# Performance work log

Measured on AMD Instinct MI355X. Metric: run time of the kernel, lower is better.

## Reference

```python
import jax, jax.numpy as jnp
import numpy as np

B, T, C, H, DH, L, V = 4096, 32, 384, 6, 64, 6, 80


def _ln(x, g, b):
    m = x.mean(-1, keepdims=True)
    v = ((x - m) ** 2).mean(-1, keepdims=True)
    return (x - m) / jnp.sqrt(v + 1e-5) * g + b


def setup_inputs() -> dict:
    key = jax.random.key(0)
    ks = jax.random.split(key, 12)
    n = lambda k, s: jax.random.normal(k, s, dtype=jnp.float32) * 0.02
    return dict(
        idx=jax.random.randint(ks[0], (B, T), 0, V),
        tok_emb=n(ks[1], (V, C)),
        pos_emb=n(ks[2], (T, C)),
        ln1_g=jnp.ones((L, C), jnp.float32), ln1_b=jnp.zeros((L, C), jnp.float32),
        Wq=n(ks[3], (L, H, C, DH)), Wk=n(ks[4], (L, H, C, DH)), Wv=n(ks[5], (L, H, C, DH)),
        Wo=n(ks[6], (L, C, C)), bo=jnp.zeros((L, C), jnp.float32),
        ln2_g=jnp.ones((L, C), jnp.float32), ln2_b=jnp.zeros((L, C), jnp.float32),
        W1=n(ks[7], (L, C, 4 * C)), b1=jnp.zeros((L, 4 * C), jnp.float32),
        W2=n(ks[8], (L, 4 * C, C)), b2=jnp.zeros((L, C), jnp.float32),
        lnf_g=jnp.ones((C,), jnp.float32), lnf_b=jnp.zeros((C,), jnp.float32),
        Wlm=n(ks[9], (C, V)), blm=jnp.zeros((V,), jnp.float32),
    )


def reference(idx, tok_emb, pos_emb, ln1_g, ln1_b, Wq, Wk, Wv, Wo, bo,
              ln2_g, ln2_b, W1, b1, W2, b2, lnf_g, lnf_b, Wlm, blm):
    # token + position embeddings
    x = tok_emb[idx] + pos_emb[None]  # [B, T, C]
    mask = jnp.tril(jnp.ones((T, T), dtype=bool))  # causal

    def block(x, p):
        l1g, l1b, wq, wk, wv, wo, b_o, l2g, l2b, w1, b_1, w2, b_2 = p
        h = _ln(x, l1g, l1b)
        q = jnp.einsum('btc,hcd->bhtd', h, wq)
        k = jnp.einsum('btc,hcd->bhtd', h, wk)
        v = jnp.einsum('btc,hcd->bhtd', h, wv)
        s = jnp.einsum('bhtd,bhsd->bhts', q, k) * (DH ** -0.5)
        s = jnp.where(mask, s, -jnp.inf)
        a = jax.nn.softmax(s, axis=-1)  # dropout is identity in eval
        o = jnp.einsum('bhts,bhsd->bhtd', a, v)
        o = o.transpose(0, 2, 1, 3).reshape(x.shape[0], T, C)  # concat heads
        x = x + o @ wo + b_o
        h2 = _ln(x, l2g, l2b)
        x = x + jax.nn.relu(h2 @ w1 + b_1) @ w2 + b_2
        return x, None

    params = (ln1_g, ln1_b, Wq, Wk, Wv, Wo, bo, ln2_g, ln2_b, W1, b1, W2, b2)
    x, _ = jax.lax.scan(block, x, params)
    x = _ln(x, lnf_g, lnf_b)
    return x @ Wlm + blm  # [B, T, V]
```

## Files before the change

kernel.cpp:

```cpp
#include <hip/hip_runtime.h>
#include <hip/hip_fp16.h>
#include <stdint.h>


typedef unsigned short u16;
typedef __bf16 bf16x8 __attribute__((ext_vector_type(8)));
typedef float f32x4 __attribute__((ext_vector_type(4)));
typedef float f32x4v __attribute__((ext_vector_type(4)));
typedef unsigned uint2v __attribute__((ext_vector_type(2)));

#define M_TOK 131072
#define CDIM  384
#define TT    32
#define HH    6
#define DHEAD 64
#define LLAY  6
#define VOCAB 80
#define FFDIM 1536
#define QKVN  1152

__device__ __forceinline__ float b2f(u16 v) {
    union { unsigned int u; float f; } x; x.u = ((unsigned int)v) << 16; return x.f;
}
__device__ __forceinline__ u16 f2b(float f) {
    union { float f; unsigned int u; } x; x.f = f;
    unsigned int r = (x.u + 0x7fffu + ((x.u >> 16) & 1u)) >> 16;
    return (u16)r;
}
__device__ __forceinline__ void gload16(const u16* g, u16* l) {
    __builtin_amdgcn_global_load_lds(
        (const __attribute__((address_space(1))) void*)g,
        (__attribute__((address_space(3))) void*)l,
        16, 0, 0);
}
__device__ __forceinline__ float load_in(const void* p, size_t i, int m) {
    if (m == 0) return ((const float*)p)[i];
    u16 v = ((const u16*)p)[i];
    if (m == 1) return b2f(v);
    __half h; *(u16*)&h = v; return __half2float(h);
}

__global__ void detect_dtype_kernel(const void* ln1g, int* flag) {
    if (threadIdx.x == 0 && blockIdx.x == 0) {
        unsigned w = *(const unsigned*)ln1g;
        int m = 0;
        if (w == 0x3F803F80u) m = 1;
        else if (w == 0x3C003C00u) m = 2;
        *flag = m;
    }
}

__global__ void cvt_kernel(const void* __restrict__ src, u16* __restrict__ dst,
                           unsigned n, const int* __restrict__ flag) {
    const int m = *flag;
    unsigned i = blockIdx.x * 256 + threadIdx.x;
    if (i < n) dst[i] = f2b(load_in(src, i, m));
}

__global__ void transpose_kernel(const void* __restrict__ src, u16* __restrict__ dst,
                                 int R, int Cc, unsigned total,
                                 const int* __restrict__ flag) {
    const int m = *flag;
    unsigned i = blockIdx.x * 256 + threadIdx.x;
    if (i >= total) return;
    unsigned c  = i % R;
    unsigned t2 = i / R;
    unsigned n  = t2 % Cc;
    unsigned l  = t2 / Cc;
    dst[i] = f2b(load_in(src, ((size_t)l * R + c) * Cc + n, m));
}

__global__ void pack_qkv_kernel(const void* __restrict__ Wq, const void* __restrict__ Wk,
                                const void* __restrict__ Wv, u16* __restrict__ dst,
                                const int* __restrict__ flag) {
    const int m = *flag;
    unsigned i = blockIdx.x * 256 + threadIdx.x;
    const unsigned total = (unsigned)LLAY * QKVN * CDIM;
    if (i >= total) return;
    unsigned c  = i % CDIM;
    unsigned t2 = i / CDIM;
    unsigned n  = t2 % QKVN;
    unsigned l  = t2 / QKVN;
    const void* W = (n < 384) ? Wq : (n < 768) ? Wk : Wv;
    unsigned nn = n % 384;
    unsigned hh = nn >> 6, d = nn & 63;
    dst[i] = f2b(load_in(W, (((size_t)l * HH + hh) * CDIM + c) * DHEAD + d, m));
}

__global__ void embed_kernel(const int* __restrict__ idx, const void* __restrict__ tok,
                             const void* __restrict__ pos, float* __restrict__ x,
                             unsigned rows0, const int* __restrict__ flag) {
    const int m = *flag;
    unsigned i = blockIdx.x * 256 + threadIdx.x;
    unsigned c  = i % CDIM;
    unsigned bt = i / CDIM + rows0;
    unsigned t  = bt & (TT - 1);
    int id = idx[bt];
    x[i] = load_in(tok, (size_t)id * CDIM + c, m) + load_in(pos, (size_t)t * CDIM + c, m);
}

__global__ __launch_bounds__(256) void ln_kernel(const float* __restrict__ x,
                                                 const u16* __restrict__ g,
                                                 const u16* __restrict__ b,
                                                 u16* __restrict__ out) {
    const unsigned row  = blockIdx.x * 4 + (threadIdx.x >> 6);
    const unsigned lane = threadIdx.x & 63;
    const float* xr = x + (size_t)row * CDIM;
    float v[6]; float s = 0.f, s2 = 0.f;
#pragma unroll
    for (int j = 0; j < 6; j++) { v[j] = xr[lane + j * 64]; s += v[j]; s2 += v[j] * v[j]; }
#pragma unroll
    for (int off = 32; off; off >>= 1) { s += __shfl_xor(s, off); s2 += __shfl_xor(s2, off); }
    float mean = s * (1.f / CDIM);
    float var  = fmaxf(s2 * (1.f / CDIM) - mean * mean, 0.f);
    float rstd = rsqrtf(var + 1e-5f);
    u16* orow = out + (size_t)row * CDIM;
#pragma unroll
    for (int j = 0; j < 6; j++) {
        unsigned c = lane + j * 64;
        orow[c] = f2b((v[j] - mean) * rstd * b2f(g[c]) + b2f(b[c]));
    }
}

template<bool WIDE, bool BIAS, bool RELU, bool RESID, bool NBOUND, bool FOUT>
__global__ __launch_bounds__(512, WIDE ? 4 : 6)
void gemm_kernel(const u16* __restrict__ A, const u16* __restrict__ Bt,
                 const u16* __restrict__ bias, const float* resid,
                 u16* __restrict__ Cb, float* Cf,
                 int N, int K, int nt) {
    constexpr int BN = WIDE ? 256 : 128;
    constexpr int NF = WIDE ? 4 : 2;
    constexpr int WC = BN / 4;
    constexpr int BI = BN / 64;
    __shared__ __align__(16) u16 smem[8192 + BN * 64];
    u16* As = smem;
    u16* Bs = smem + 8192;
    float* eps = (float*)smem;

    const int tid  = threadIdx.x;
    const int lane = tid & 63;
    const int w    = tid >> 6;
    const int quad = lane >> 4;
    const int l16  = lane & 15;
    const int wm = w >> 2, wn = w & 3;

    const int id = blockIdx.x;
    const int sgrp = id >> 3;
    const int mtile = (id & 7) + 8 * (sgrp / nt);
    const int ntile = sgrp % nt;
    const long m0 = (long)mtile * 128;
    const long n0 = (long)ntile * BN;

    const u16* Ag[2]; u16* ldsA[2];
    const u16* Bg[BI]; u16* ldsB[BI];
#pragma unroll
    for (int n = 0; n < 2; n++) {
        const int si  = w * 128 + n * 64 + lane;
        const int row = si >> 3;
        const int p   = si & 7;
        const int s   = p ^ (row & 7);
        Ag[n] = A + (size_t)(m0 + row) * K + s * 8;
        ldsA[n] = As + (size_t)(w * 128 + n * 64) * 8;
    }
#pragma unroll
    for (int n = 0; n < BI; n++) {
        const int si  = (w * BI + n) * 64 + lane;
        const int row = si >> 3;
        const int p   = si & 7;
        const int s   = p ^ (row & 7);
        long brow = n0 + row;
        if (NBOUND) brow = brow < N ? brow : N - 1;
        Bg[n] = Bt + (size_t)brow * K + s * 8;
        ldsB[n] = Bs + (size_t)((w * BI + n) * 64) * 8;
    }

    f32x4 acc[4][NF];
#pragma unroll
    for (int i = 0; i < 4; i++)
#pragma unroll
        for (int j = 0; j < NF; j++) acc[i][j] = f32x4{0.f, 0.f, 0.f, 0.f};

    for (int k0 = 0; k0 < K; k0 += 64) {
        __syncthreads();
#pragma unroll
        for (int n = 0; n < 2; n++)  gload16(Ag[n] + k0, ldsA[n]);
#pragma unroll
        for (int n = 0; n < BI; n++) gload16(Bg[n] + k0, ldsB[n]);
        __syncthreads();
#pragma unroll
        for (int k32 = 0; k32 < 2; k32++) {
            bf16x8 af[4], bfr[NF];
#pragma unroll
            for (int i = 0; i < 4; i++) {
                const int row = wm * 64 + i * 16 + l16;
                const int p   = (k32 * 4 + quad) ^ (row & 7);
                af[i] = *(const bf16x8*)(&As[row * 64 + p * 8]);
            }
#pragma unroll
            for (int j = 0; j < NF; j++) {
                const int row = wn * WC + j * 16 + l16;
                const int p   = (k32 * 4 + quad) ^ (row & 7);
                bfr[j] = *(const bf16x8*)(&Bs[row * 64 + p * 8]);
            }
#pragma unroll
            for (int i = 0; i < 4; i++)
#pragma unroll
                for (int j = 0; j < NF; j++)
                    acc[i][j] = __builtin_amdgcn_mfma_f32_16x16x32_bf16(af[i], bfr[j], acc[i][j], 0, 0, 0);
        }
    }

    float bv[NF];
#pragma unroll
    for (int j = 0; j < NF; j++) {
        if (BIAS) {
            int col = (int)n0 + wn * WC + j * 16 + l16;
            bv[j] = (!NBOUND || col < N) ? b2f(bias[col]) : 0.f;
        } else bv[j] = 0.f;
    }

    constexpr int SR  = WIDE ? 32 : 64;
    constexpr int NPH = 128 / SR;
    constexpr int IB  = SR / 16;
    constexpr int TPR = BN / 4;
    constexpr int RPP = 512 / TPR;
    const int cc = (tid & (TPR - 1)) * 4;
    const int rr = tid / TPR;
#pragma unroll
    for (int q = 0; q < NPH; q++) {
        __syncthreads();
        if (wm == (q * SR) / 64) {
            const int ibase = ((q * SR) % 64) / 16;
#pragma unroll
            for (int ii = 0; ii < IB; ii++)
#pragma unroll
                for (int j = 0; j < NF; j++) {
                    const int lr = ii * 16 + quad * 4;
                    const int lc = wn * WC + j * 16 + l16;
#pragma unroll
                    for (int r = 0; r < 4; r++) {
                        float v = acc[ibase + ii][j][r] + bv[j];
                        if (RELU) v = fmaxf(v, 0.f);
                        eps[(lr + r) * BN + lc] = v;
                    }
                }
        }
        __syncthreads();
        const long rowbase = m0 + q * SR;
#pragma unroll
        for (int p = 0; p < SR / RPP; p++) {
            const int lrow = p * RPP + rr;
            const long grow = rowbase + lrow;
            f32x4v v = *(const f32x4v*)&eps[lrow * BN + cc];
            const long col = n0 + cc;
            if (RESID) {
                if (!NBOUND || col + 3 < N) {
                    const f32x4v rv = *(const f32x4v*)&resid[grow * N + col];
                    v = v + rv;
                    __builtin_nontemporal_store(v, (f32x4v*)&Cf[grow * N + col]);
                }
            } else if (FOUT) {
                if (!NBOUND || col + 3 < N)
                    __builtin_nontemporal_store(v, (f32x4v*)&Cf[grow * N + col]);
            } else {
                if (!NBOUND || col + 3 < N) {
                    uint2v pk;
                    pk.x = (unsigned)f2b(v.x) | ((unsigned)f2b(v.y) << 16);
                    pk.y = (unsigned)f2b(v.z) | ((unsigned)f2b(v.w) << 16);
                    __builtin_nontemporal_store(pk, (uint2v*)&Cb[grow * N + col]);
                }
            }
        }
    }
}

__global__ __launch_bounds__(256, 2) void attn_kernel(const u16* __restrict__ qkv,
                                                      u16* __restrict__ o) {
    __shared__ __align__(16) u16 alds[4 * 3840];
    const int w    = threadIdx.x >> 6;
    u16* Pl = alds + w * 3840;
    u16* VT = Pl + 1280;

    const int gw   = blockIdx.x * 4 + w;
    const int seq  = gw / HH;
    const int h    = gw - seq * HH;
    const int lane = threadIdx.x & 63;
    const int l16  = lane & 15;
    const int quad = lane >> 4;

    const u16* base = qkv + (size_t)seq * TT * QKVN;
    const u16* Qb = base + h * DHEAD;
    const u16* Kb = base + 384 + h * DHEAD;
    const u16* Vb = base + 768 + h * DHEAD;

    {
        const int s  = lane & 31;
        const int hf = lane >> 5;
#pragma unroll
        for (int c = 0; c < 4; c++) {
            uint4 v = *(const uint4*)(Vb + (size_t)s * QKVN + hf * 32 + c * 8);
            const u16* pv = (const u16*)&v;
#pragma unroll
            for (int j = 0; j < 8; j++) {
                const int d = hf * 32 + c * 8 + j;
                VT[d * 40 + s] = pv[j];
            }
        }
    }

    bf16x8 qf[2][2], kf[2][2];
#pragma unroll
    for (int ti = 0; ti < 2; ti++)
#pragma unroll
        for (int kt = 0; kt < 2; kt++)
            qf[ti][kt] = *(const bf16x8*)(Qb + (size_t)(ti * 16 + l16) * QKVN + kt * 32 + quad * 8);
#pragma unroll
    for (int si = 0; si < 2; si++)
#pragma unroll
        for (int kt = 0; kt < 2; kt++)
            kf[si][kt] = *(const bf16x8*)(Kb + (size_t)(si * 16 + l16) * QKVN + kt * 32 + quad * 8);

    f32x4 S00 = f32x4{0.f, 0.f, 0.f, 0.f};
    f32x4 S10 = f32x4{0.f, 0.f, 0.f, 0.f};
    f32x4 S11 = f32x4{0.f, 0.f, 0.f, 0.f};
#pragma unroll
    for (int kt = 0; kt < 2; kt++) {
        S00 = __builtin_amdgcn_mfma_f32_16x16x32_bf16(qf[0][kt], kf[0][kt], S00, 0, 0, 0);
        S10 = __builtin_amdgcn_mfma_f32_16x16x32_bf16(qf[1][kt], kf[0][kt], S10, 0, 0, 0);
        S11 = __builtin_amdgcn_mfma_f32_16x16x32_bf16(qf[1][kt], kf[1][kt], S11, 0, 0, 0);
    }

#pragma unroll
    for (int ti = 0; ti < 2; ti++) {
#pragma unroll
        for (int r = 0; r < 4; r++) {
            const int t = ti * 16 + quad * 4 + r;
            float v0 = (ti ? S10[r] : S00[r]) * 0.125f;
            if (l16 > t) v0 = -1e30f;
            float v1 = -1e30f;
            if (ti == 1) {
                v1 = S11[r] * 0.125f;
                if (16 + l16 > t) v1 = -1e30f;
            }
            float m = fmaxf(v0, v1);
#pragma unroll
            for (int k = 1; k < 16; k <<= 1) m = fmaxf(m, __shfl_xor(m, k));
            const float e0 = __expf(v0 - m);
            const float e1 = (ti == 1) ? __expf(v1 - m) : 0.f;
            float l = e0 + e1;
#pragma unroll
            for (int k = 1; k < 16; k <<= 1) l += __shfl_xor(l, k);
            const float inv = 1.f / l;
            Pl[t * 40 + l16]      = f2b(e0 * inv);
            Pl[t * 40 + 16 + l16] = f2b(e1 * inv);
        }
    }

    bf16x8 pf[2], vf[4];
#pragma unroll
    for (int ti = 0; ti < 2; ti++)
        pf[ti] = *(const bf16x8*)(&Pl[(ti * 16 + l16) * 40 + quad * 8]);
#pragma unroll
    for (int dt = 0; dt < 4; dt++)
        vf[dt] = *(const bf16x8*)(&VT[(dt * 16 + l16) * 40 + quad * 8]);

    u16* ob = o + ((size_t)seq * TT) * CDIM + h * DHEAD;
#pragma unroll
    for (int ti = 0; ti < 2; ti++) {
#pragma unroll
        for (int dt = 0; dt < 4; dt++) {
            f32x4 O2 = f32x4{0.f, 0.f, 0.f, 0.f};
            O2 = __builtin_amdgcn_mfma_f32_16x16x32_bf16(pf[ti], vf[dt], O2, 0, 0, 0);
#pragma unroll
            for (int r = 0; r < 4; r++) {
                const int t = ti * 16 + quad * 4 + r;
                ob[(size_t)t * CDIM + dt * 16 + l16] = f2b(O2[r]);
            }
        }
    }
}

extern "C" void kernel_launch(void* const* d_in, const int* in_sizes, int n_in,
                              void* d_out, int out_size, void* d_ws, size_t ws_size,
                              hipStream_t stream) {
    const int*  idx  = (const int*)d_in[0];
    const void* tok  = d_in[1];
    const void* pos  = d_in[2];
    const void* ln1g = d_in[3];
    const void* ln1b = d_in[4];
    const void* Wq   = d_in[5];
    const void* Wk   = d_in[6];
    const void* Wv   = d_in[7];
    const void* Wo   = d_in[8];
    const void* bo   = d_in[9];
    const void* ln2g = d_in[10];
    const void* ln2b = d_in[11];
    const void* W1   = d_in[12];
    const void* b1   = d_in[13];
    const void* W2   = d_in[14];
    const void* b2   = d_in[15];
    const void* lnfg = d_in[16];
    const void* lnfb = d_in[17];
    const void* Wlm  = d_in[18];
    const void* blm  = d_in[19];

    const size_t wq_b  = (size_t)LLAY * QKVN * CDIM * 2;
    const size_t wo_b  = (size_t)LLAY * CDIM * CDIM * 2;
    const size_t w1_b  = (size_t)LLAY * FFDIM * CDIM * 2;
    const size_t w2_b  = (size_t)LLAY * CDIM * FFDIM * 2;
    const size_t wlm_b = (size_t)VOCAB * CDIM * 2;
    const size_t wts   = wq_b + wo_b + w1_b + w2_b + wlm_b;

    const unsigned P_LN1G = 0,      P_LN1B = 2304,  P_BO  = 4608;
    const unsigned P_LN2G = 6912,   P_LN2B = 9216,  P_B1  = 11520;
    const unsigned P_B2   = 20736,  P_LNFG = 23040, P_LNFB = 23424;
    const unsigned P_BLM  = 23808,  P_TOT  = 23888;
    const size_t pbuf_b = ((size_t)P_TOT * 2 + 255) & ~(size_t)255;

    int NC = 32;
    {
        const int cand[6] = {1, 2, 4, 8, 16, 32};
        for (int ci = 0; ci < 6; ci++) {
            size_t rows_c = (size_t)M_TOK / cand[ci];
            size_t need = rows_c * 5376 + wts + pbuf_b + 4096;
            if (need <= ws_size) { NC = cand[ci]; break; }
        }
    }
    const size_t rows = (size_t)M_TOK / NC;
    const int mt = (int)(rows / 128);

    char* ws = (char*)d_ws;
    size_t off = 0;
    float* x    = (float*)(ws + off); off += rows * CDIM * 4;
    u16*   h    = (u16*)(ws + off);   off += rows * CDIM * 2;
    char*  S    = ws + off;           off += rows * 3072;
    u16*   qkv  = (u16*)S;
    u16*   o    = (u16*)(S + rows * QKVN * 2);
    u16*   u    = (u16*)S;
    u16* wqkvT  = (u16*)(ws + off);   off += wq_b;
    u16* woT    = (u16*)(ws + off);   off += wo_b;
    u16* w1T    = (u16*)(ws + off);   off += w1_b;
    u16* w2T    = (u16*)(ws + off);   off += w2_b;
    u16* wlmT   = (u16*)(ws + off);   off += wlm_b;
    u16* pbuf   = (u16*)(ws + off);   off += pbuf_b;
    int* flag   = (int*)(ws + off);   off += 256;

    detect_dtype_kernel<<<1, 64, 0, stream>>>(ln1g, flag);

    struct { const void* src; unsigned doff, n; } cv[10] = {
        { ln1g, P_LN1G, 2304 }, { ln1b, P_LN1B, 2304 }, { bo, P_BO, 2304 },
        { ln2g, P_LN2G, 2304 }, { ln2b, P_LN2B, 2304 }, { b1, P_B1, 9216 },
        { b2,   P_B2,   2304 }, { lnfg, P_LNFG, 384 },  { lnfb, P_LNFB, 384 },
        { blm,  P_BLM,  80 },
    };
    for (int i = 0; i < 10; i++)
        cvt_kernel<<<(cv[i].n + 255) / 256, 256, 0, stream>>>(cv[i].src, pbuf + cv[i].doff, cv[i].n, flag);

    {
        unsigned tq = (unsigned)LLAY * QKVN * CDIM;
        pack_qkv_kernel<<<(tq + 255) / 256, 256, 0, stream>>>(Wq, Wk, Wv, wqkvT, flag);
        unsigned t1 = (unsigned)LLAY * CDIM * CDIM;
        transpose_kernel<<<(t1 + 255) / 256, 256, 0, stream>>>(Wo, woT, CDIM, CDIM, t1, flag);
        unsigned t2t = (unsigned)LLAY * CDIM * FFDIM;
        transpose_kernel<<<(t2t + 255) / 256, 256, 0, stream>>>(W1, w1T, CDIM, FFDIM, t2t, flag);
        transpose_kernel<<<(t2t + 255) / 256, 256, 0, stream>>>(W2, w2T, FFDIM, CDIM, t2t, flag);
        unsigned t3 = (unsigned)VOCAB * CDIM;
        transpose_kernel<<<(t3 + 255) / 256, 256, 0, stream>>>(Wlm, wlmT, CDIM, VOCAB, t3, flag);
    }

    for (int c = 0; c < NC; c++) {
        const size_t r0 = c * rows;
        embed_kernel<<<(rows * CDIM) / 256, 256, 0, stream>>>(idx, tok, pos, x, (unsigned)r0, flag);

        for (int l = 0; l < LLAY; l++) {
            ln_kernel<<<rows / 4, 256, 0, stream>>>(x, pbuf + P_LN1G + l * CDIM, pbuf + P_LN1B + l * CDIM, h);
            gemm_kernel<true, false, false, false, true, false><<<mt * 5, 512, 0, stream>>>(
                h, wqkvT + (size_t)l * QKVN * CDIM, nullptr, nullptr, qkv, nullptr, QKVN, CDIM, 5);
            attn_kernel<<<(rows / TT) * HH / 4, 256, 0, stream>>>(qkv, o);
            gemm_kernel<false, true, false, true, false, false><<<mt * 3, 512, 0, stream>>>(
                o, woT + (size_t)l * CDIM * CDIM, pbuf + P_BO + l * CDIM, x, nullptr, x, CDIM, CDIM, 3);
            ln_kernel<<<rows / 4, 256, 0, stream>>>(x, pbuf + P_LN2G + l * CDIM, pbuf + P_LN2B + l * CDIM, h);
            gemm_kernel<true, true, true, false, false, false><<<mt * 6, 512, 0, stream>>>(
                h, w1T + (size_t)l * FFDIM * CDIM, pbuf + P_B1 + l * FFDIM, nullptr, u, nullptr, FFDIM, CDIM, 6);
            gemm_kernel<false, true, false, true, false, false><<<mt * 3, 512, 0, stream>>>(
                u, w2T + (size_t)l * CDIM * FFDIM, pbuf + P_B2 + l * CDIM, x, nullptr, x, CDIM, FFDIM, 3);
        }

        ln_kernel<<<rows / 4, 256, 0, stream>>>(x, pbuf + P_LNFG, pbuf + P_LNFB, h);
        gemm_kernel<false, true, false, false, true, true><<<mt, 512, 0, stream>>>(
            h, wlmT, pbuf + P_BLM, nullptr, nullptr, (float*)d_out + r0 * VOCAB, VOCAB, CDIM, 1);
    }
}
```

Before: 5.872 ms.

## Fuse FFN up and down projections into one kernel keeping hidden activations on-chip

Replaces the two FFN GEMM launches with a single kernel per 128-row tile. It computes the ReLU hidden activations 64 columns at a time in shared memory and immediately accumulates them into the down-projection registers, adding bias and residual at the end. This removes the global write and read of the 1536-wide intermediate. In exchange it uses a large shared-memory footprint (160KB) and many synchronizations per chunk without double buffering, and it launches only one block per 128 rows, so occupancy and parallelism drop.

```diff
diff --git a/kernel.cpp b/kernel.cpp
--- a/kernel.cpp
+++ b/kernel.cpp
@@ -270,6 +270,155 @@
                     __builtin_nontemporal_store(pk, (uint2v*)&Cb[grow * N + col]);
                 }
             }
+        }
+    }
+}
+
+__global__ __launch_bounds__(512, 2)
+void ffn_kernel(const u16* __restrict__ hh, const u16* __restrict__ W1t,
+                const u16* __restrict__ W2t, const u16* __restrict__ b1,
+                const u16* __restrict__ b2, float* __restrict__ x) {
+    __shared__ __align__(16) u16 smem[81920];
+    u16* hs  = smem;
+    u16* us  = smem + 49152;
+    u16* wsb = smem + 57344;
+    float* eps = (float*)smem;
+
+    const int tid  = threadIdx.x;
+    const int lane = tid & 63;
+    const int w    = tid >> 6;
+    const int quad = lane >> 4;
+    const int l16  = lane & 15;
+    const int wm = w >> 2, wn = w & 3;
+    const long m0 = (long)blockIdx.x * 128;
+
+#pragma unroll
+    for (int j = 0; j < 12; j++) {
+        const int L   = j * 512 + w * 64 + lane;
+        const int row = L / 48;
+        const int sl  = L % 48;
+        const int gs  = (sl & ~7) | ((sl & 7) ^ (row & 7));
+        gload16(hh + (size_t)(m0 + row) * 384 + gs * 8,
+                hs + (size_t)(j * 512 + w * 64) * 8);
+    }
+
+    f32x4 accx[4][6];
+#pragma unroll
+    for (int i = 0; i < 4; i++)
+#pragma unroll
+        for (int j = 0; j < 6; j++) accx[i][j] = f32x4{0.f, 0.f, 0.f, 0.f};
+
+    const float b1base = 0.f; (void)b1base;
+
+    for (int ch = 0; ch < 24; ch++) {
+        if (ch) __syncthreads();
+#pragma unroll
+        for (int j = 0; j < 6; j++) {
+            const int L   = j * 512 + w * 64 + lane;
+            const int row = L / 48;
+            const int sl  = L % 48;
+            const int gs  = (sl & ~7) | ((sl & 7) ^ (row & 7));
+            gload16(W1t + (size_t)(ch * 64 + row) * 384 + gs * 8,
+                    wsb + (size_t)(j * 512 + w * 64) * 8);
+        }
+        __syncthreads();
+
+        f32x4 accu[4];
+#pragma unroll
+        for (int mf = 0; mf < 4; mf++) accu[mf] = f32x4{0.f, 0.f, 0.f, 0.f};
+#pragma unroll
+        for (int kk = 0; kk < 12; kk++) {
+            const int s0 = kk * 4 + quad;
+            bf16x8 bf;
+            {
+                const int n = wn * 16 + l16;
+                const int s = (s0 & ~7) | ((s0 & 7) ^ (n & 7));
+                bf = *(const bf16x8*)(&wsb[n * 384 + s * 8]);
+            }
+#pragma unroll
+            for (int mf = 0; mf < 4; mf++) {
+                const int row = wm * 64 + mf * 16 + l16;
+                const int s   = (s0 & ~7) | ((s0 & 7) ^ (row & 7));
+                const bf16x8 af = *(const bf16x8*)(&hs[row * 384 + s * 8]);
+                accu[mf] = __builtin_amdgcn_mfma_f32_16x16x32_bf16(af, bf, accu[mf], 0, 0, 0);
+            }
+        }
+        {
+            const int col = wn * 16 + l16;
+            const float b1v = b2f(b1[ch * 64 + col]);
+#pragma unroll
+            for (int mf = 0; mf < 4; mf++)
+#pragma unroll
+                for (int r = 0; r < 4; r++) {
+                    const int row = wm * 64 + mf * 16 + quad * 4 + r;
+                    const int ps  = (col >> 3) ^ (row & 7);
+                    us[row * 64 + ps * 8 + (col & 7)] =
+                        f2b(fmaxf(accu[mf][r] + b1v, 0.f));
+                }
+        }
+        __syncthreads();
+#pragma unroll
+        for (int j = 0; j < 6; j++) {
+            const int si  = j * 512 + w * 64 + lane;
+            const int row = si >> 3;
+            const int s   = (si & 7) ^ (row & 7);
+            gload16(W2t + (size_t)row * 1536 + ch * 64 + s * 8,
+                    wsb + (size_t)(j * 512 + w * 64) * 8);
+        }
+        __syncthreads();
+
+#pragma unroll
+        for (int kk2 = 0; kk2 < 2; kk2++) {
+            bf16x8 uf[4], wf[6];
+#pragma unroll
+            for (int mf = 0; mf < 4; mf++) {
+                const int row = wm * 64 + mf * 16 + l16;
+                const int p   = (kk2 * 4 + quad) ^ (row & 7);
+                uf[mf] = *(const bf16x8*)(&us[row * 64 + p * 8]);
+            }
+#pragma unroll
+            for (int j = 0; j < 6; j++) {
+                const int n = wn * 96 + j * 16 + l16;
+                const int p = (kk2 * 4 + quad) ^ (n & 7);
+                wf[j] = *(const bf16x8*)(&wsb[n * 64 + p * 8]);
+            }
+#pragma unroll
+            for (int mf = 0; mf < 4; mf++)
+#pragma unroll
+                for (int j = 0; j < 6; j++)
+                    accx[mf][j] = __builtin_amdgcn_mfma_f32_16x16x32_bf16(uf[mf], wf[j], accx[mf][j], 0, 0, 0);
+        }
+    }
+
+    float b2v[6];
+#pragma unroll
+    for (int j = 0; j < 6; j++) b2v[j] = b2f(b2[wn * 96 + j * 16 + l16]);
+#pragma unroll
+    for (int q = 0; q < 2; q++) {
+        __syncthreads();
+        if (wm == q) {
+#pragma unroll
+            for (int mf = 0; mf < 4; mf++)
+#pragma unroll
+                for (int j = 0; j < 6; j++) {
+                    const int lr = mf * 16 + quad * 4;
+                    const int lc = wn * 96 + j * 16 + l16;
+#pragma unroll
+                    for (int r = 0; r < 4; r++)
+                        eps[(lr + r) * 384 + lc] = accx[mf][j][r] + b2v[j];
+                }
+        }
+        __syncthreads();
+        const long rowbase = m0 + q * 64;
+#pragma unroll
+        for (int p = 0; p < 12; p++) {
+            const int idxp = p * 512 + tid;
+            const int row  = idxp / 96;
+            const int c4   = (idxp % 96) * 4;
+            f32x4v v = *(const f32x4v*)&eps[row * 384 + c4];
+            const f32x4v rv = *(const f32x4v*)&x[(rowbase + row) * 384 + c4];
+            v = v + rv;
+            __builtin_nontemporal_store(v, (f32x4v*)&x[(rowbase + row) * 384 + c4]);
         }
     }
 }
@@ -436,7 +585,6 @@
     char*  S    = ws + off;           off += rows * 3072;
     u16*   qkv  = (u16*)S;
     u16*   o    = (u16*)(S + rows * QKVN * 2);
-    u16*   u    = (u16*)S;
     u16* wqkvT  = (u16*)(ws + off);   off += wq_b;
     u16* woT    = (u16*)(ws + off);   off += wo_b;
     u16* w1T    = (u16*)(ws + off);   off += w1_b;
@@ -480,10 +628,9 @@
             gemm_kernel<false, true, false, true, false, false><<<mt * 3, 512, 0, stream>>>(
                 o, woT + (size_t)l * CDIM * CDIM, pbuf + P_BO + l * CDIM, x, nullptr, x, CDIM, CDIM, 3);
             ln_kernel<<<rows / 4, 256, 0, stream>>>(x, pbuf + P_LN2G + l * CDIM, pbuf + P_LN2B + l * CDIM, h);
-            gemm_kernel<true, true, true, false, false, false><<<mt * 6, 512, 0, stream>>>(
-                h, w1T + (size_t)l * FFDIM * CDIM, pbuf + P_B1 + l * FFDIM, nullptr, u, nullptr, FFDIM, CDIM, 6);
-            gemm_kernel<false, true, false, true, false, false><<<mt * 3, 512, 0, stream>>>(
-                u, w2T + (size_t)l * CDIM * FFDIM, pbuf + P_B2 + l * CDIM, x, nullptr, x, CDIM, FFDIM, 3);
+            ffn_kernel<<<mt, 512, 0, stream>>>(
+                h, w1T + (size_t)l * FFDIM * CDIM, w2T + (size_t)l * CDIM * FFDIM,
+                pbuf + P_B1 + l * FFDIM, pbuf + P_B2 + l * CDIM, x);
         }
 
         ln_kernel<<<rows / 4, 256, 0, stream>>>(x, pbuf + P_LNFG, pbuf + P_LNFB, h);
```

New measurement: 6.288 ms. 7.1% more time.

## Triple-buffer GEMM K-loop with async prefetch and vmcnt-based waits

Applied to the files above, without the earlier changes.

Restructures the GEMM main loop into a 3-stage LDS ring with 32-wide K tiles. Global-to-LDS loads run two tiles ahead, and fine-grained s_waitcnt vmcnt plus raw s_barrier replace the two __syncthreads per iteration. The change also drops the XOR swizzle on the LDS layout, raises wave priority around the MFMA block, and unifies launch bounds to 4. The aim is to hide global load latency behind MFMA work. The risks are LDS bank conflicts from the unswizzled layout, more LDS use lowering occupancy, and more barriers per unit of K work.

```diff
diff --git a/kernel.cpp b/kernel.cpp
--- a/kernel.cpp
+++ b/kernel.cpp
@@ -123,18 +123,17 @@
 }
 
 template<bool WIDE, bool BIAS, bool RELU, bool RESID, bool NBOUND, bool FOUT>
-__global__ __launch_bounds__(512, WIDE ? 4 : 6)
+__global__ __launch_bounds__(512, 4)
 void gemm_kernel(const u16* __restrict__ A, const u16* __restrict__ Bt,
                  const u16* __restrict__ bias, const float* resid,
                  u16* __restrict__ Cb, float* Cf,
                  int N, int K, int nt) {
-    constexpr int BN = WIDE ? 256 : 128;
-    constexpr int NF = WIDE ? 4 : 2;
-    constexpr int WC = BN / 4;
-    constexpr int BI = BN / 64;
-    __shared__ __align__(16) u16 smem[8192 + BN * 64];
-    u16* As = smem;
-    u16* Bs = smem + 8192;
+    constexpr int BN  = WIDE ? 256 : 128;
+    constexpr int NF  = WIDE ? 4 : 2;
+    constexpr int WC  = BN / 4;
+    constexpr int BJ  = WIDE ? 2 : 1;
+    constexpr int BUF = 4096 + BN * 32;
+    __shared__ __align__(16) u16 smem[3 * BUF];
     float* eps = (float*)smem;
 
     const int tid  = threadIdx.x;
@@ -151,27 +150,20 @@
     const long m0 = (long)mtile * 128;
     const long n0 = (long)ntile * BN;
 
-    const u16* Ag[2]; u16* ldsA[2];
-    const u16* Bg[BI]; u16* ldsB[BI];
-#pragma unroll
-    for (int n = 0; n < 2; n++) {
-        const int si  = w * 128 + n * 64 + lane;
-        const int row = si >> 3;
-        const int p   = si & 7;
-        const int s   = p ^ (row & 7);
-        Ag[n] = A + (size_t)(m0 + row) * K + s * 8;
-        ldsA[n] = As + (size_t)(w * 128 + n * 64) * 8;
-    }
-#pragma unroll
-    for (int n = 0; n < BI; n++) {
-        const int si  = (w * BI + n) * 64 + lane;
-        const int row = si >> 3;
-        const int p   = si & 7;
-        const int s   = p ^ (row & 7);
+    const int arow = tid >> 2, as_ = tid & 3;
+    const u16* Ag = A + (size_t)(m0 + arow) * K + as_ * 8;
+    const int aoff = (w * 64) * 8;
+
+    const u16* Bg[BJ]; int boff[BJ];
+#pragma unroll
+    for (int j = 0; j < BJ; j++) {
+        const int si  = j * 512 + tid;
+        const int row = si >> 2;
+        const int s   = si & 3;
         long brow = n0 + row;
         if (NBOUND) brow = brow < N ? brow : N - 1;
-        Bg[n] = Bt + (size_t)brow * K + s * 8;
-        ldsB[n] = Bs + (size_t)((w * BI + n) * 64) * 8;
+        Bg[j]   = Bt + (size_t)brow * K + s * 8;
+        boff[j] = 4096 + (j * 512 + w * 64) * 8;
     }
 
     f32x4 acc[4][NF];
@@ -180,34 +172,61 @@
 #pragma unroll
         for (int j = 0; j < NF; j++) acc[i][j] = f32x4{0.f, 0.f, 0.f, 0.f};
 
-    for (int k0 = 0; k0 < K; k0 += 64) {
-        __syncthreads();
-#pragma unroll
-        for (int n = 0; n < 2; n++)  gload16(Ag[n] + k0, ldsA[n]);
-#pragma unroll
-        for (int n = 0; n < BI; n++) gload16(Bg[n] + k0, ldsB[n]);
-        __syncthreads();
-#pragma unroll
-        for (int k32 = 0; k32 < 2; k32++) {
-            bf16x8 af[4], bfr[NF];
-#pragma unroll
-            for (int i = 0; i < 4; i++) {
-                const int row = wm * 64 + i * 16 + l16;
-                const int p   = (k32 * 4 + quad) ^ (row & 7);
-                af[i] = *(const bf16x8*)(&As[row * 64 + p * 8]);
-            }
-#pragma unroll
-            for (int j = 0; j < NF; j++) {
-                const int row = wn * WC + j * 16 + l16;
-                const int p   = (k32 * 4 + quad) ^ (row & 7);
-                bfr[j] = *(const bf16x8*)(&Bs[row * 64 + p * 8]);
-            }
-#pragma unroll
-            for (int i = 0; i < 4; i++)
-#pragma unroll
-                for (int j = 0; j < NF; j++)
-                    acc[i][j] = __builtin_amdgcn_mfma_f32_16x16x32_bf16(af[i], bfr[j], acc[i][j], 0, 0, 0);
-        }
+    const int KT = K >> 5;
+
+#pragma unroll
+    for (int t = 0; t < 2; t++) {
+        u16* buf = smem + t * BUF;
+        gload16(Ag + t * 32, buf + aoff);
+#pragma unroll
+        for (int j = 0; j < BJ; j++) gload16(Bg[j] + t * 32, buf + boff[j]);
+    }
+
+    for (int t = 0; t < KT; t++) {
+        if (t + 2 < KT) {
+            u16* buf = smem + ((t + 2) % 3) * BUF;
+            const int k0 = (t + 2) * 32;
+            gload16(Ag + k0, buf + aoff);
+#pragma unroll
+            for (int j = 0; j < BJ; j++) gload16(Bg[j] + k0, buf + boff[j]);
+        }
+        const int rem = KT - 1 - t;
+        if (rem >= 2) {
+            if constexpr (WIDE) asm volatile("s_waitcnt vmcnt(6)" ::: "memory");
+            else                asm volatile("s_waitcnt vmcnt(4)" ::: "memory");
+        } else if (rem == 1) {
+            if constexpr (WIDE) asm volatile("s_waitcnt vmcnt(3)" ::: "memory");
+            else                asm volatile("s_waitcnt vmcnt(2)" ::: "memory");
+        } else {
+            asm volatile("s_waitcnt vmcnt(0)" ::: "memory");
+        }
+        __builtin_amdgcn_s_barrier();
+        __builtin_amdgcn_sched_barrier(0);
+
+        const u16* As = smem + (t % 3) * BUF;
+        const u16* Bs = As + 4096;
+        bf16x8 af[4], bfr[NF];
+#pragma unroll
+        for (int i = 0; i < 4; i++) {
+            const int row = wm * 64 + i * 16 + l16;
+            af[i] = *(const bf16x8*)(&As[row * 32 + quad * 8]);
+        }
+#pragma unroll
+        for (int j = 0; j < NF; j++) {
+            const int row = wn * WC + j * 16 + l16;
+            bfr[j] = *(const bf16x8*)(&Bs[row * 32 + quad * 8]);
+        }
+        asm volatile("s_waitcnt lgkmcnt(0)" ::: "memory");
+        __builtin_amdgcn_sched_barrier(0);
+        __builtin_amdgcn_s_barrier();
+
+        __builtin_amdgcn_s_setprio(1);
+#pragma unroll
+        for (int i = 0; i < 4; i++)
+#pragma unroll
+            for (int j = 0; j < NF; j++)
+                acc[i][j] = __builtin_amdgcn_mfma_f32_16x16x32_bf16(af[i], bfr[j], acc[i][j], 0, 0, 0);
+        __builtin_amdgcn_s_setprio(0);
     }
 
     float bv[NF];
```

Measured after the change: 6.193 ms. +5.5%, slower.

## Fuse LayerNorm into the A-operand load of the following GEMMs

Applied to the files above, without the earlier changes.

Removes the standalone LayerNorm kernels and the bf16 h buffer. The QKV, FFN-up and LM-head GEMMs now read the fp32 residual stream directly, compute per-row mean and rstd in a prologue, and normalize each K-tile into LDS with the swizzled layout. The aim is to cut a full write and read of the normalized activations plus the launch overhead. In exchange, every N-tile block recomputes the row statistics and reads fp32 instead of bf16 (the QKV GEMM has 5 N-tiles and FFN-up has 6), and A is loaded synchronously through registers instead of the async gload. Launch bounds are also changed to a uniform occupancy hint of 4.

```diff
diff --git a/kernel.cpp b/kernel.cpp
--- a/kernel.cpp
+++ b/kernel.cpp
@@ -99,32 +99,11 @@
     x[i] = load_in(tok, (size_t)id * CDIM + c, m) + load_in(pos, (size_t)t * CDIM + c, m);
 }
 
-__global__ __launch_bounds__(256) void ln_kernel(const float* __restrict__ x,
-                                                 const u16* __restrict__ g,
-                                                 const u16* __restrict__ b,
-                                                 u16* __restrict__ out) {
-    const unsigned row  = blockIdx.x * 4 + (threadIdx.x >> 6);
-    const unsigned lane = threadIdx.x & 63;
-    const float* xr = x + (size_t)row * CDIM;
-    float v[6]; float s = 0.f, s2 = 0.f;
-#pragma unroll
-    for (int j = 0; j < 6; j++) { v[j] = xr[lane + j * 64]; s += v[j]; s2 += v[j] * v[j]; }
-#pragma unroll
-    for (int off = 32; off; off >>= 1) { s += __shfl_xor(s, off); s2 += __shfl_xor(s2, off); }
-    float mean = s * (1.f / CDIM);
-    float var  = fmaxf(s2 * (1.f / CDIM) - mean * mean, 0.f);
-    float rstd = rsqrtf(var + 1e-5f);
-    u16* orow = out + (size_t)row * CDIM;
-#pragma unroll
-    for (int j = 0; j < 6; j++) {
-        unsigned c = lane + j * 64;
-        orow[c] = f2b((v[j] - mean) * rstd * b2f(g[c]) + b2f(b[c]));
-    }
-}
-
-template<bool WIDE, bool BIAS, bool RELU, bool RESID, bool NBOUND, bool FOUT>
-__global__ __launch_bounds__(512, WIDE ? 4 : 6)
-void gemm_kernel(const u16* __restrict__ A, const u16* __restrict__ Bt,
+template<bool WIDE, bool BIAS, bool RELU, bool RESID, bool NBOUND, bool FOUT, bool LNA>
+__global__ __launch_bounds__(512, 4)
+void gemm_kernel(const u16* __restrict__ A, const float* __restrict__ Ax,
+                 const u16* __restrict__ lng, const u16* __restrict__ lnb,
+                 const u16* __restrict__ Bt,
                  const u16* __restrict__ bias, const float* resid,
                  u16* __restrict__ Cb, float* Cf,
                  int N, int K, int nt) {
@@ -152,16 +131,39 @@
     const long n0 = (long)ntile * BN;
 
     const u16* Ag[2]; u16* ldsA[2];
+    if constexpr (!LNA) {
+#pragma unroll
+        for (int n = 0; n < 2; n++) {
+            const int si  = w * 128 + n * 64 + lane;
+            const int row = si >> 3;
+            const int p   = si & 7;
+            const int s   = p ^ (row & 7);
+            Ag[n] = A + (size_t)(m0 + row) * K + s * 8;
+            ldsA[n] = As + (size_t)(w * 128 + n * 64) * 8;
+        }
+    }
+    const int arow = tid >> 2, acg = tid & 3;
+    const float* xrow = LNA ? (Ax + (size_t)(m0 + arow) * CDIM) : nullptr;
+    float gmean = 0.f, grstd = 0.f;
+    f32x4v xv[4];
+    if constexpr (LNA) {
+        float s = 0.f, s2 = 0.f;
+#pragma unroll
+        for (int i = 0; i < 24; i++) {
+            const f32x4v v = *(const f32x4v*)&xrow[acg * 96 + i * 4];
+            s  += v.x + v.y + v.z + v.w;
+            s2 += v.x * v.x + v.y * v.y + v.z * v.z + v.w * v.w;
+        }
+        s += __shfl_xor(s, 1); s2 += __shfl_xor(s2, 1);
+        s += __shfl_xor(s, 2); s2 += __shfl_xor(s2, 2);
+        gmean = s * (1.f / CDIM);
+        grstd = rsqrtf(fmaxf(s2 * (1.f / CDIM) - gmean * gmean, 0.f) + 1e-5f);
+#pragma unroll
+        for (int i = 0; i < 4; i++)
+            xv[i] = *(const f32x4v*)&xrow[acg * 16 + i * 4];
+    }
+
     const u16* Bg[BI]; u16* ldsB[BI];
-#pragma unroll
-    for (int n = 0; n < 2; n++) {
-        const int si  = w * 128 + n * 64 + lane;
-        const int row = si >> 3;
-        const int p   = si & 7;
-        const int s   = p ^ (row & 7);
-        Ag[n] = A + (size_t)(m0 + row) * K + s * 8;
-        ldsA[n] = As + (size_t)(w * 128 + n * 64) * 8;
-    }
 #pragma unroll
     for (int n = 0; n < BI; n++) {
         const int si  = (w * BI + n) * 64 + lane;
@@ -182,10 +184,40 @@
 
     for (int k0 = 0; k0 < K; k0 += 64) {
         __syncthreads();
-#pragma unroll
-        for (int n = 0; n < 2; n++)  gload16(Ag[n] + k0, ldsA[n]);
+        if constexpr (LNA) {
+            const uint4 gv0 = *(const uint4*)(lng + k0 + acg * 16);
+            const uint4 gv1 = *(const uint4*)(lng + k0 + acg * 16 + 8);
+            const uint4 bv0 = *(const uint4*)(lnb + k0 + acg * 16);
+            const uint4 bv1 = *(const uint4*)(lnb + k0 + acg * 16 + 8);
+            u16 ga[16], ba[16];
+            *(uint4*)&ga[0] = gv0; *(uint4*)&ga[8] = gv1;
+            *(uint4*)&ba[0] = bv0; *(uint4*)&ba[8] = bv1;
+            unsigned pw[8];
+#pragma unroll
+            for (int ii = 0; ii < 8; ii++) {
+                const int c0 = ii * 2, c1 = c0 + 1;
+                const float h0 = (xv[c0 >> 2][c0 & 3] - gmean) * grstd * b2f(ga[c0]) + b2f(ba[c0]);
+                const float h1 = (xv[c1 >> 2][c1 & 3] - gmean) * grstd * b2f(ga[c1]) + b2f(ba[c1]);
+                pw[ii] = (unsigned)f2b(h0) | ((unsigned)f2b(h1) << 16);
+            }
+            const int s0 = acg * 2, s1 = s0 + 1;
+            uint4 pa; pa.x = pw[0]; pa.y = pw[1]; pa.z = pw[2]; pa.w = pw[3];
+            uint4 pb; pb.x = pw[4]; pb.y = pw[5]; pb.z = pw[6]; pb.w = pw[7];
+            *(uint4*)&As[arow * 64 + ((s0 ^ (arow & 7)) * 8)] = pa;
+            *(uint4*)&As[arow * 64 + ((s1 ^ (arow & 7)) * 8)] = pb;
+        } else {
+#pragma unroll
+            for (int n = 0; n < 2; n++) gload16(Ag[n] + k0, ldsA[n]);
+        }
 #pragma unroll
         for (int n = 0; n < BI; n++) gload16(Bg[n] + k0, ldsB[n]);
+        if constexpr (LNA) {
+            if (k0 + 64 < K) {
+#pragma unroll
+                for (int i = 0; i < 4; i++)
+                    xv[i] = *(const f32x4v*)&xrow[k0 + 64 + acg * 16 + i * 4];
+            }
+        }
         __syncthreads();
 #pragma unroll
         for (int k32 = 0; k32 < 2; k32++) {
@@ -432,7 +464,7 @@
     char* ws = (char*)d_ws;
     size_t off = 0;
     float* x    = (float*)(ws + off); off += rows * CDIM * 4;
-    u16*   h    = (u16*)(ws + off);   off += rows * CDIM * 2;
+    off += rows * CDIM * 2;
     char*  S    = ws + off;           off += rows * 3072;
     u16*   qkv  = (u16*)S;
     u16*   o    = (u16*)(S + rows * QKVN * 2);
@@ -473,21 +505,23 @@
         embed_kernel<<<(rows * CDIM) / 256, 256, 0, stream>>>(idx, tok, pos, x, (unsigned)r0, flag);
 
         for (int l = 0; l < LLAY; l++) {
-            ln_kernel<<<rows / 4, 256, 0, stream>>>(x, pbuf + P_LN1G + l * CDIM, pbuf + P_LN1B + l * CDIM, h);
-            gemm_kernel<true, false, false, false, true, false><<<mt * 5, 512, 0, stream>>>(
-                h, wqkvT + (size_t)l * QKVN * CDIM, nullptr, nullptr, qkv, nullptr, QKVN, CDIM, 5);
+            gemm_kernel<true, false, false, false, true, false, true><<<mt * 5, 512, 0, stream>>>(
+                nullptr, x, pbuf + P_LN1G + l * CDIM, pbuf + P_LN1B + l * CDIM,
+                wqkvT + (size_t)l * QKVN * CDIM, nullptr, nullptr, qkv, nullptr, QKVN, CDIM, 5);
             attn_kernel<<<(rows / TT) * HH / 4, 256, 0, stream>>>(qkv, o);
-            gemm_kernel<false, true, false, true, false, false><<<mt * 3, 512, 0, stream>>>(
-                o, woT + (size_t)l * CDIM * CDIM, pbuf + P_BO + l * CDIM, x, nullptr, x, CDIM, CDIM, 3);
-            ln_kernel<<<rows / 4, 256, 0, stream>>>(x, pbuf + P_LN2G + l * CDIM, pbuf + P_LN2B + l * CDIM, h);
-            gemm_kernel<true, true, true, false, false, false><<<mt * 6, 512, 0, stream>>>(
-                h, w1T + (size_t)l * FFDIM * CDIM, pbuf + P_B1 + l * FFDIM, nullptr, u, nullptr, FFDIM, CDIM, 6);
-            gemm_kernel<false, true, false, true, false, false><<<mt * 3, 512, 0, stream>>>(
-                u, w2T + (size_t)l * CDIM * FFDIM, pbuf + P_B2 + l * CDIM, x, nullptr, x, CDIM, FFDIM, 3);
-        }
-
-        ln_kernel<<<rows / 4, 256, 0, stream>>>(x, pbuf + P_LNFG, pbuf + P_LNFB, h);
-        gemm_kernel<false, true, false, false, true, true><<<mt, 512, 0, stream>>>(
-            h, wlmT, pbuf + P_BLM, nullptr, nullptr, (float*)d_out + r0 * VOCAB, VOCAB, CDIM, 1);
-    }
-}
+            gemm_kernel<false, true, false, true, false, false, false><<<mt * 3, 512, 0, stream>>>(
+                o, nullptr, nullptr, nullptr,
+                woT + (size_t)l * CDIM * CDIM, pbuf + P_BO + l * CDIM, x, nullptr, x, CDIM, CDIM, 3);
+            gemm_kernel<true, true, true, false, false, false, true><<<mt * 6, 512, 0, stream>>>(
+                nullptr, x, pbuf + P_LN2G + l * CDIM, pbuf + P_LN2B + l * CDIM,
+                w1T + (size_t)l * FFDIM * CDIM, pbuf + P_B1 + l * FFDIM, nullptr, u, nullptr, FFDIM, CDIM, 6);
+            gemm_kernel<false, true, false, true, false, false, false><<<mt * 3, 512, 0, stream>>>(
+                u, nullptr, nullptr, nullptr,
+                w2T + (size_t)l * CDIM * FFDIM, pbuf + P_B2 + l * CDIM, x, nullptr, x, CDIM, FFDIM, 3);
+        }
+
+        gemm_kernel<false, true, false, false, true, true, true><<<mt, 512, 0, stream>>>(
+            nullptr, x, pbuf + P_LNFG, pbuf + P_LNFB,
+            wlmT, pbuf + P_BLM, nullptr, nullptr, (float*)d_out + r0 * VOCAB, VOCAB, CDIM, 1);
+    }
+}
```

After: 8.076 ms. 1.38x slower.
